# Optimization experiments

Hardware: AMD Instinct MI355X
Metric: run time of the kernel (lower is better)

The kernel has to match this reference:

```python
import jax, jax.numpy as jnp
import numpy as np

N = 100000
E = 1600000
IN_F = 128
OUT_F = 32
HEADS = 6
NEG_SLOPE = 0.2


def setup_inputs() -> dict:
    key = jax.random.key(0)
    k1, k2, k3, k4, k5 = jax.random.split(key, 5)
    x = jax.random.normal(k1, (N, IN_F), dtype=jnp.float32)
    edge_index = jax.random.randint(k2, (2, E), 0, N, dtype=jnp.int64)
    # GATConv params (PyG layout): shared linear for src/dst, per-head attention vectors, bias
    glorot = lambda k, shape: jax.random.normal(k, shape, dtype=jnp.float32) * np.sqrt(2.0 / (shape[0] + shape[-1]))
    W = glorot(k3, (IN_F, HEADS * OUT_F))          # lin.weight^T
    att_src = glorot(k4, (HEADS, OUT_F)) * 0.1     # [H, C]
    att_dst = glorot(k5, (HEADS, OUT_F)) * 0.1
    bias = jnp.zeros((OUT_F,), dtype=jnp.float32)  # concat=False -> bias of size out_feature
    return {"x": x, "edge_index": edge_index, "W": W,
            "att_src": att_src, "att_dst": att_dst, "bias": bias}


def reference(x, edge_index, W, att_src, att_dst, bias):
    src, dst = edge_index[0], edge_index[1]
    # Linear projection to per-head features: [N, H, C]
    xp = (x @ W).reshape(N, HEADS, OUT_F)
    # Per-node attention logit halves: [N, H]
    a_s = jnp.einsum("nhc,hc->nh", xp, att_src)
    a_d = jnp.einsum("nhc,hc->nh", xp, att_dst)
    # Per-edge logits with LeakyReLU: [E, H]
    e = jax.nn.leaky_relu(a_s[src] + a_d[dst], negative_slope=NEG_SLOPE)
    # Segment softmax over edges grouped by destination node
    m = jax.ops.segment_max(e, dst, num_segments=N)            # [N, H]
    m = jnp.where(jnp.isfinite(m), m, 0.0)                     # empty segments -> -inf guard
    e = jnp.exp(e - m[dst])
    s = jax.ops.segment_sum(e, dst, num_segments=N)            # [N, H]
    alpha = e / (s[dst] + 1e-16)                               # [E, H]
    # Weighted scatter-add aggregation: [N, H, C]
    msg = xp[src] * alpha[:, :, None]
    out = jax.ops.segment_sum(msg, dst, num_segments=N)
    # concat=False -> mean over heads, add bias, then SELU
    out = out.mean(axis=1) + bias
    return jax.nn.selu(out)
```

## Files before the change

### kernel.cpp

```cpp
#include <hip/hip_runtime.h>


typedef __attribute__((ext_vector_type(8))) short short8;
typedef __attribute__((ext_vector_type(4))) float f32x4;

#define SK 136
#define SLOTS 48

__device__ __forceinline__ unsigned short f2bf(float f)
{
    unsigned int u = __float_as_uint(f);
    u = (u + 0x7fffu + ((u >> 16) & 1u)) >> 16;
    return (unsigned short)u;
}

__global__ __launch_bounds__(256) void k_prep(
    const float* __restrict__ W,
    const float* __restrict__ att_src, const float* __restrict__ att_dst,
    unsigned short* __restrict__ watT, unsigned short* __restrict__ WbT,
    int* __restrict__ deg, int N)
{
    int i = blockIdx.x * 256 + threadIdx.x;
    if (i < N) deg[i] = 0;
    if (i < 128 * 192) {
        int k = i / 192, c = i - k * 192;
        WbT[c * 128 + k] = f2bf(W[i]);
    }
    if (i < 128 * 16) {
        int k = i >> 4, c = i & 15;
        float v = 0.f;
        if (c < 12) {
            int h = c < 6 ? c : c - 6;
            const float* av = (c < 6 ? att_src : att_dst) + h * 32;
            const float* wr = W + k * 192 + h * 32;
            #pragma unroll
            for (int j = 0; j < 32; ++j) v = fmaf(wr[j], av[j], v);
        }
        watT[c * 128 + k] = f2bf(v);
    }
}

__global__ __launch_bounds__(256) void k_gd(
    const float* __restrict__ x, const unsigned short* __restrict__ WbT,
    const unsigned short* __restrict__ watT,
    unsigned char* __restrict__ xpb, float2* __restrict__ asc,
    float* __restrict__ a_d,
    const int* __restrict__ ei, int* __restrict__ deg, int* __restrict__ csr,
    int N, int E, int GB, int DB)
{
    __shared__ __align__(16) unsigned short xt[64 * SK];
    __shared__ unsigned int smax[64 * 6];
    const int t   = threadIdx.x;
    const int bid = (int)blockIdx.x >> 1;

    if (blockIdx.x & 1) {
        if (bid >= DB) return;
        const int G = DB * 256;
        const int gid = bid * 256 + t;
        int s[4], d[4], r[4];
        #pragma unroll
        for (int k = 0; k < 4; ++k) {
            int e = gid + k * G;
            bool ok = e < E;
            int ec = ok ? e : 0;
            s[k] = ei[ec];
            d[k] = ei[E + ec];
            if (!ok) d[k] = -1;
        }
        #pragma unroll
        for (int k = 0; k < 4; ++k)
            r[k] = (d[k] >= 0) ? atomicAdd(&deg[d[k]], 1) : SLOTS;
        #pragma unroll
        for (int k = 0; k < 4; ++k)
            if (r[k] < SLOTS && d[k] >= 0) csr[d[k] * SLOTS + r[k]] = s[k];
        return;
    }

    if (bid >= GB) return;
    const int wave = t >> 6;
    const int lane = t & 63;
    const int ln   = lane & 15;
    const int q    = lane >> 4;
    const int n0   = bid * 64;
    const int cb   = wave * 48;

    {
        const float4* x4 = (const float4*)x;
        #pragma unroll
        for (int it = 0; it < 8; ++it) {
            int i   = t + it * 256;
            int row = i >> 5;
            int c4  = i & 31;
            int gr  = n0 + row;
            if (gr > N - 1) gr = N - 1;
            float4 f = x4[(size_t)gr * 32 + c4];
            unsigned int u0 = (unsigned int)f2bf(f.x) | ((unsigned int)f2bf(f.y) << 16);
            unsigned int u1 = (unsigned int)f2bf(f.z) | ((unsigned int)f2bf(f.w) << 16);
            *(uint2*)(xt + row * SK + c4 * 4) = make_uint2(u0, u1);
        }
        if (t < 128) { smax[t] = 0u; smax[t + 128] = 0u; smax[t + 256] = 0u; }
    }

    short8 bw[3][4];
    #pragma unroll
    for (int nt = 0; nt < 3; ++nt)
        #pragma unroll
        for (int kbi = 0; kbi < 4; ++kbi)
            bw[nt][kbi] = *(const short8*)(WbT + (cb + nt * 16 + ln) * 128
                                               + kbi * 32 + q * 8);
    short8 bwa[4];
    #pragma unroll
    for (int kbi = 0; kbi < 4; ++kbi)
        bwa[kbi] = *(const short8*)(watT + ln * 128 + kbi * 32 + q * 8);

    __syncthreads();

    f32x4 acc[4][3];
    #pragma unroll
    for (int mt = 0; mt < 4; ++mt)
        #pragma unroll
        for (int nt = 0; nt < 3; ++nt) acc[mt][nt] = (f32x4)0.f;

    #pragma unroll
    for (int kbi = 0; kbi < 4; ++kbi) {
        #pragma unroll
        for (int mt = 0; mt < 4; ++mt) {
            short8 av = *(const short8*)(xt + (mt * 16 + ln) * SK + kbi * 32 + q * 8);
            #pragma unroll
            for (int nt = 0; nt < 3; ++nt)
                acc[mt][nt] = __builtin_amdgcn_mfma_f32_16x16x32_bf16(
                    av, bw[nt][kbi], acc[mt][nt], 0, 0, 0);
        }
    }

    f32x4 acca = (f32x4)0.f;
    #pragma unroll
    for (int kbi = 0; kbi < 4; ++kbi) {
        short8 av = *(const short8*)(xt + (wave * 16 + ln) * SK + kbi * 32 + q * 8);
        acca = __builtin_amdgcn_mfma_f32_16x16x32_bf16(av, bwa[kbi], acca, 0, 0, 0);
    }

    #pragma unroll
    for (int mt = 0; mt < 4; ++mt) {
        #pragma unroll
        for (int r = 0; r < 4; ++r) {
            int row = mt * 16 + q * 4 + r;
            #pragma unroll
            for (int nt = 0; nt < 3; ++nt) {
                float m = fabsf(acc[mt][nt][r]);
                #pragma unroll
                for (int d = 1; d <= 8; d <<= 1)
                    m = fmaxf(m, __shfl_xor(m, d));
                if (ln == 0) {
                    int head = (cb + nt * 16) >> 5;
                    atomicMax(&smax[row * 6 + head], __float_as_uint(m));
                }
            }
        }
    }
    #pragma unroll
    for (int r = 0; r < 4; ++r) {
        int grow = n0 + wave * 16 + q * 4 + r;
        if (grow < N) {
            if (ln < 6)       asc[(size_t)grow * 6 + ln].x   = acca[r];
            else if (ln < 12) a_d[(size_t)grow * 6 + ln - 6] = acca[r];
        }
    }
    __syncthreads();

    for (int i2 = t; i2 < 384; i2 += 256) {
        int row = i2 / 6, h = i2 - row * 6;
        float m = __uint_as_float(smax[i2]);
        int grow = n0 + row;
        if (grow < N) asc[(size_t)grow * 6 + h].y = m * (1.f / 127.f);
        smax[i2] = __float_as_uint(m > 0.f ? 127.f / m : 0.f);
    }
    __syncthreads();

    #pragma unroll
    for (int mt = 0; mt < 4; ++mt) {
        #pragma unroll
        for (int r = 0; r < 4; ++r) {
            int row  = mt * 16 + q * 4 + r;
            int grow = n0 + row;
            if (grow < N) {
                #pragma unroll
                for (int nt = 0; nt < 3; ++nt) {
                    int head = (cb + nt * 16) >> 5;
                    float inv = __uint_as_float(smax[row * 6 + head]);
                    int qv = (int)rintf(acc[mt][nt][r] * inv) + 128;
                    xpb[(size_t)grow * 192 + cb + nt * 16 + ln] = (unsigned char)qv;
                }
            }
        }
    }
}

__global__ __launch_bounds__(256) void k_agg(
    const unsigned char* __restrict__ xpb, const float2* __restrict__ asc,
    const float* __restrict__ a_d,
    const int* __restrict__ csr, const int* __restrict__ degv,
    const float* __restrict__ bias, float* __restrict__ out, int N)
{
    const int wid = threadIdx.x >> 6;
    const int l   = threadIdx.x & 63;
    const int n = blockIdx.x * 4 + wid;
    if (n >= N) return;

    int deg = degv[n];
    deg = deg < SLOTS ? deg : SLOTS;
    const int nb  = n * SLOTS;
    const int hr  = l >> 3;
    const int h   = hr < 6 ? hr : 5;
    const int lc  = l < 48 ? l : 47;
    const unsigned lcb = (unsigned)lc * 4u;
    const unsigned h8  = (unsigned)h * 8u;
    const char* __restrict__ xpB  = (const char*)xpb;
    const char* __restrict__ ascB = (const char*)asc;

    const float zd = a_d[(size_t)n * 6 + h];

    float ax = 0.f, ay = 0.f, az = 0.f, aw = 0.f, se = 0.f, sevs = 0.f;

    int my3 = (l < deg) ? csr[nb + l] * 3 : 0;
    int i = 0;
    for (; i + 8 <= deg; i += 8) {
        unsigned s3[8]; float2 av[8]; unsigned int xv[8];
        #pragma unroll
        for (int k = 0; k < 8; ++k) {
            s3[k] = (unsigned)__shfl(my3, i + k);
            av[k] = *(const float2*)(ascB + s3[k] * 16u + h8);
        }
        #pragma unroll
        for (int k = 0; k < 8; ++k)
            xv[k] = *(const unsigned int*)(xpB + s3[k] * 64u + lcb);
        #pragma unroll
        for (int k = 0; k < 8; ++k) {
            float z = av[k].x + zd;
            z = fmaxf(z, 0.2f * z);
            float ev = __expf(z);
            float evs = ev * av[k].y;
            unsigned v = xv[k];
            float f0 = (float)(v & 0xffu);
            float f1 = (float)((v >> 8) & 0xffu);
            float f2 = (float)((v >> 16) & 0xffu);
            float f3 = (float)(v >> 24);
            ax = fmaf(evs, f0, ax);
            ay = fmaf(evs, f1, ay);
            az = fmaf(evs, f2, az);
            aw = fmaf(evs, f3, aw);
            se += ev;
            sevs += evs;
        }
    }
    for (; i < deg; ++i) {
        unsigned s3 = (unsigned)__shfl(my3, i);
        float2 av = *(const float2*)(ascB + s3 * 16u + h8);
        float z = av.x + zd;
        z = fmaxf(z, 0.2f * z);
        float ev = __expf(z);
        float evs = ev * av.y;
        unsigned v = *(const unsigned int*)(xpB + s3 * 64u + lcb);
        float f0 = (float)(v & 0xffu);
        float f1 = (float)((v >> 8) & 0xffu);
        float f2 = (float)((v >> 16) & 0xffu);
        float f3 = (float)(v >> 24);
        ax = fmaf(evs, f0, ax);
        ay = fmaf(evs, f1, ay);
        az = fmaf(evs, f2, az);
        aw = fmaf(evs, f3, aw);
        se += ev;
        sevs += evs;
    }

    const float cor = 128.f * sevs;
    const float inv = 1.f / (se + 1e-16f);
    float v0 = (l < 48) ? (ax - cor) * inv : 0.f;
    float v1 = (l < 48) ? (ay - cor) * inv : 0.f;
    float v2 = (l < 48) ? (az - cor) * inv : 0.f;
    float v3 = (l < 48) ? (aw - cor) * inv : 0.f;

    #pragma unroll
    for (int d = 8; d <= 32; d <<= 1) {
        v0 += __shfl_down(v0, d);
        v1 += __shfl_down(v1, d);
        v2 += __shfl_down(v2, d);
        v3 += __shfl_down(v3, d);
    }

    if (l < 8) {
        float4 b4 = ((const float4*)bias)[l];
        const float scs = 1.0507009873554805f, al = 1.6732632423543772f;
        float m[4] = {v0 * (1.f / 6.f) + b4.x, v1 * (1.f / 6.f) + b4.y,
                      v2 * (1.f / 6.f) + b4.z, v3 * (1.f / 6.f) + b4.w};
        #pragma unroll
        for (int k = 0; k < 4; ++k)
            m[k] = m[k] > 0.f ? scs * m[k] : scs * al * (__expf(m[k]) - 1.f);
        ((float4*)out)[(size_t)n * 8 + l] = make_float4(m[0], m[1], m[2], m[3]);
    }
}

extern "C" void kernel_launch(void* const* d_in, const int* in_sizes, int n_in,
                              void* d_out, int out_size, void* d_ws, size_t ws_size,
                              hipStream_t stream)
{
    const float* x       = (const float*)d_in[0];
    const int*   ei      = (const int*)d_in[1];
    const float* W       = (const float*)d_in[2];
    const float* att_src = (const float*)d_in[3];
    const float* att_dst = (const float*)d_in[4];
    const float* bias    = (const float*)d_in[5];
    float* out = (float*)d_out;

    const int N = in_sizes[0] / 128;
    const int E = in_sizes[1] / 2;
    const int GB = (N + 63) / 64;
    const int DB = (E + 4 * 256 - 1) / (4 * 256);
    const int MB = (GB > DB ? GB : DB) * 2;

    char* ws = (char*)d_ws;
    size_t o = 0;
    auto take = [&](size_t bytes) { size_t r = o; o = (o + bytes + 255) & ~(size_t)255; return r; };
    unsigned char* xpb = (unsigned char*)(ws + take((size_t)N * 192));
    float2* asc    = (float2*)(ws + take((size_t)N * 6 * 8));
    float*  a_d    = (float*) (ws + take((size_t)N * 6 * 4));
    int*    deg    = (int*)   (ws + take((size_t)N * 4));
    int*    csr    = (int*)   (ws + take((size_t)N * SLOTS * 4));
    unsigned short* watT = (unsigned short*)(ws + take((size_t)128 * 16 * 2));
    unsigned short* WbT  = (unsigned short*)(ws + take((size_t)128 * 192 * 2));
    (void)ws_size; (void)n_in; (void)out_size;

    int pg = (N + 255) / 256;
    k_prep<<<pg, 256, 0, stream>>>(W, att_src, att_dst, watT, WbT, deg, N);
    k_gd<<<MB, 256, 0, stream>>>(x, WbT, watT, xpb, asc, a_d,
                                 ei, deg, csr, N, E, GB, DB);
    k_agg<<<(N + 3) / 4, 256, 0, stream>>>(xpb, asc, a_d, csr, deg, bias, out, N);
}
```

Measured before the change: 272.6 us.

## Use six waves per GEMM block so each wave owns one head

The projection/degree kernel now runs 384 threads per block, so each of six waves computes exactly one 32-column head (two 16-wide N tiles) instead of four waves covering 48 columns each. Because a wave owns a whole head, the per-row absmax for int8 quantization is reduced entirely with shuffles inside the wave. This removes the shared-memory atomicMax table and two block barriers. The attention-logit MFMA is limited to the first four waves, and the degree-counting half is resized to 384 threads per block. The larger block and the per-wave shuffle work may change occupancy.

Result: no change. 276.3 us (+1.4%).

```diff
diff --git a/kernel.cpp b/kernel.cpp
--- a/kernel.cpp
+++ b/kernel.cpp
@@ -40,7 +40,7 @@
     }
 }
 
-__global__ __launch_bounds__(256) void k_gd(
+__global__ __launch_bounds__(384) void k_gd(
     const float* __restrict__ x, const unsigned short* __restrict__ WbT,
     const unsigned short* __restrict__ watT,
     unsigned char* __restrict__ xpb, float2* __restrict__ asc,
@@ -49,14 +49,13 @@
     int N, int E, int GB, int DB)
 {
     __shared__ __align__(16) unsigned short xt[64 * SK];
-    __shared__ unsigned int smax[64 * 6];
     const int t   = threadIdx.x;
     const int bid = (int)blockIdx.x >> 1;
 
     if (blockIdx.x & 1) {
         if (bid >= DB) return;
-        const int G = DB * 256;
-        const int gid = bid * 256 + t;
+        const int G = DB * 384;
+        const int gid = bid * 384 + t;
         int s[4], d[4], r[4];
         #pragma unroll
         for (int k = 0; k < 4; ++k) {
@@ -82,44 +81,47 @@
     const int ln   = lane & 15;
     const int q    = lane >> 4;
     const int n0   = bid * 64;
-    const int cb   = wave * 48;
+    const int cb   = wave * 32;
 
     {
         const float4* x4 = (const float4*)x;
         #pragma unroll
-        for (int it = 0; it < 8; ++it) {
-            int i   = t + it * 256;
-            int row = i >> 5;
-            int c4  = i & 31;
-            int gr  = n0 + row;
-            if (gr > N - 1) gr = N - 1;
-            float4 f = x4[(size_t)gr * 32 + c4];
-            unsigned int u0 = (unsigned int)f2bf(f.x) | ((unsigned int)f2bf(f.y) << 16);
-            unsigned int u1 = (unsigned int)f2bf(f.z) | ((unsigned int)f2bf(f.w) << 16);
-            *(uint2*)(xt + row * SK + c4 * 4) = make_uint2(u0, u1);
-        }
-        if (t < 128) { smax[t] = 0u; smax[t + 128] = 0u; smax[t + 256] = 0u; }
-    }
-
-    short8 bw[3][4];
-    #pragma unroll
-    for (int nt = 0; nt < 3; ++nt)
+        for (int it = 0; it < 6; ++it) {
+            int i = t + it * 384;
+            if (i < 2048) {
+                int row = i >> 5;
+                int c4  = i & 31;
+                int gr  = n0 + row;
+                if (gr > N - 1) gr = N - 1;
+                float4 f = x4[(size_t)gr * 32 + c4];
+                unsigned int u0 = (unsigned int)f2bf(f.x) | ((unsigned int)f2bf(f.y) << 16);
+                unsigned int u1 = (unsigned int)f2bf(f.z) | ((unsigned int)f2bf(f.w) << 16);
+                *(uint2*)(xt + row * SK + c4 * 4) = make_uint2(u0, u1);
+            }
+        }
+    }
+
+    short8 bw[2][4];
+    #pragma unroll
+    for (int nt = 0; nt < 2; ++nt)
         #pragma unroll
         for (int kbi = 0; kbi < 4; ++kbi)
             bw[nt][kbi] = *(const short8*)(WbT + (cb + nt * 16 + ln) * 128
                                                + kbi * 32 + q * 8);
     short8 bwa[4];
-    #pragma unroll
-    for (int kbi = 0; kbi < 4; ++kbi)
-        bwa[kbi] = *(const short8*)(watT + ln * 128 + kbi * 32 + q * 8);
+    if (wave < 4) {
+        #pragma unroll
+        for (int kbi = 0; kbi < 4; ++kbi)
+            bwa[kbi] = *(const short8*)(watT + ln * 128 + kbi * 32 + q * 8);
+    }
 
     __syncthreads();
 
-    f32x4 acc[4][3];
+    f32x4 acc[4][2];
     #pragma unroll
     for (int mt = 0; mt < 4; ++mt)
         #pragma unroll
-        for (int nt = 0; nt < 3; ++nt) acc[mt][nt] = (f32x4)0.f;
+        for (int nt = 0; nt < 2; ++nt) acc[mt][nt] = (f32x4)0.f;
 
     #pragma unroll
     for (int kbi = 0; kbi < 4; ++kbi) {
@@ -127,67 +129,44 @@
         for (int mt = 0; mt < 4; ++mt) {
             short8 av = *(const short8*)(xt + (mt * 16 + ln) * SK + kbi * 32 + q * 8);
             #pragma unroll
-            for (int nt = 0; nt < 3; ++nt)
+            for (int nt = 0; nt < 2; ++nt)
                 acc[mt][nt] = __builtin_amdgcn_mfma_f32_16x16x32_bf16(
                     av, bw[nt][kbi], acc[mt][nt], 0, 0, 0);
         }
     }
 
-    f32x4 acca = (f32x4)0.f;
-    #pragma unroll
-    for (int kbi = 0; kbi < 4; ++kbi) {
-        short8 av = *(const short8*)(xt + (wave * 16 + ln) * SK + kbi * 32 + q * 8);
-        acca = __builtin_amdgcn_mfma_f32_16x16x32_bf16(av, bwa[kbi], acca, 0, 0, 0);
+    if (wave < 4) {
+        f32x4 acca = (f32x4)0.f;
+        #pragma unroll
+        for (int kbi = 0; kbi < 4; ++kbi) {
+            short8 av = *(const short8*)(xt + (wave * 16 + ln) * SK + kbi * 32 + q * 8);
+            acca = __builtin_amdgcn_mfma_f32_16x16x32_bf16(av, bwa[kbi], acca, 0, 0, 0);
+        }
+        #pragma unroll
+        for (int r = 0; r < 4; ++r) {
+            int grow = n0 + wave * 16 + q * 4 + r;
+            if (grow < N) {
+                if (ln < 6)       asc[(size_t)grow * 6 + ln].x   = acca[r];
+                else if (ln < 12) a_d[(size_t)grow * 6 + ln - 6] = acca[r];
+            }
+        }
     }
 
     #pragma unroll
     for (int mt = 0; mt < 4; ++mt) {
         #pragma unroll
         for (int r = 0; r < 4; ++r) {
-            int row = mt * 16 + q * 4 + r;
+            float m = fmaxf(fabsf(acc[mt][0][r]), fabsf(acc[mt][1][r]));
             #pragma unroll
-            for (int nt = 0; nt < 3; ++nt) {
-                float m = fabsf(acc[mt][nt][r]);
-                #pragma unroll
-                for (int d = 1; d <= 8; d <<= 1)
-                    m = fmaxf(m, __shfl_xor(m, d));
-                if (ln == 0) {
-                    int head = (cb + nt * 16) >> 5;
-                    atomicMax(&smax[row * 6 + head], __float_as_uint(m));
-                }
-            }
-        }
-    }
-    #pragma unroll
-    for (int r = 0; r < 4; ++r) {
-        int grow = n0 + wave * 16 + q * 4 + r;
-        if (grow < N) {
-            if (ln < 6)       asc[(size_t)grow * 6 + ln].x   = acca[r];
-            else if (ln < 12) a_d[(size_t)grow * 6 + ln - 6] = acca[r];
-        }
-    }
-    __syncthreads();
-
-    for (int i2 = t; i2 < 384; i2 += 256) {
-        int row = i2 / 6, h = i2 - row * 6;
-        float m = __uint_as_float(smax[i2]);
-        int grow = n0 + row;
-        if (grow < N) asc[(size_t)grow * 6 + h].y = m * (1.f / 127.f);
-        smax[i2] = __float_as_uint(m > 0.f ? 127.f / m : 0.f);
-    }
-    __syncthreads();
-
-    #pragma unroll
-    for (int mt = 0; mt < 4; ++mt) {
-        #pragma unroll
-        for (int r = 0; r < 4; ++r) {
+            for (int d = 1; d <= 8; d <<= 1)
+                m = fmaxf(m, __shfl_xor(m, d));
             int row  = mt * 16 + q * 4 + r;
             int grow = n0 + row;
             if (grow < N) {
+                float inv = m > 0.f ? 127.f / m : 0.f;
+                if (ln == 0) asc[(size_t)grow * 6 + wave].y = m * (1.f / 127.f);
                 #pragma unroll
-                for (int nt = 0; nt < 3; ++nt) {
-                    int head = (cb + nt * 16) >> 5;
-                    float inv = __uint_as_float(smax[row * 6 + head]);
+                for (int nt = 0; nt < 2; ++nt) {
                     int qv = (int)rintf(acc[mt][nt][r] * inv) + 128;
                     xpb[(size_t)grow * 192 + cb + nt * 16 + ln] = (unsigned char)qv;
                 }
@@ -315,7 +294,7 @@
     const int N = in_sizes[0] / 128;
     const int E = in_sizes[1] / 2;
     const int GB = (N + 63) / 64;
-    const int DB = (E + 4 * 256 - 1) / (4 * 256);
+    const int DB = (E + 4 * 384 - 1) / (4 * 384);
     const int MB = (GB > DB ? GB : DB) * 2;
 
     char* ws = (char*)d_ws;
@@ -332,7 +311,7 @@
 
     int pg = (N + 255) / 256;
     k_prep<<<pg, 256, 0, stream>>>(W, att_src, att_dst, watT, WbT, deg, N);
-    k_gd<<<MB, 256, 0, stream>>>(x, WbT, watT, xpb, asc, a_d,
+    k_gd<<<MB, 384, 0, stream>>>(x, WbT, watT, xpb, asc, a_d,
                                  ei, deg, csr, N, E, GB, DB);
     k_agg<<<(N + 3) / 4, 256, 0, stream>>>(xpb, asc, a_d, csr, deg, bias, out, N);
 }
```
